# Optimization experiments

Measured on AMD Instinct MI355X. Metric: run time of the kernel, lower is better.

Reference implementation:

```python
import jax, jax.numpy as jnp
import numpy as np

GROUP = 32
HEADS = 8
EPS = 1e-5


def setup_inputs() -> dict:
    key = jax.random.key(0)
    k1, k2, k3 = jax.random.split(key, 3)
    C = 512
    x = jax.random.normal(k1, (8, C, 32, 32), dtype=jnp.float32)
    gn_w = jnp.ones((C,), dtype=jnp.float32)
    gn_b = jnp.zeros((C,), dtype=jnp.float32)
    # 1x1 convs == channel matmuls; init like torch conv default (kaiming-ish scale)
    w_qkv = jax.random.normal(k2, (3 * C, C), dtype=jnp.float32) * (1.0 / np.sqrt(C))
    w_proj = jax.random.normal(k3, (C, C), dtype=jnp.float32) * (1.0 / np.sqrt(C))
    return {"x": x, "gn_w": gn_w, "gn_b": gn_b, "w_qkv": w_qkv, "w_proj": w_proj}


def _forward(x, gn_w, gn_b, w_qkv, w_proj):
    B, C, H, W = x.shape
    N = H * W
    d = C // HEADS
    scale = d ** -0.5
    # GroupNorm over (channels_per_group, H, W)
    xg = x.reshape(B, GROUP, C // GROUP, H, W)
    mean = xg.mean(axis=(2, 3, 4), keepdims=True)
    var = xg.var(axis=(2, 3, 4), keepdims=True)
    xn = ((xg - mean) * jax.lax.rsqrt(var + EPS)).reshape(B, C, H, W)
    xn = xn * gn_w[None, :, None, None] + gn_b[None, :, None, None]
    # 1x1 conv QKV: [3C, C] x [B, C, H, W]
    qkv = jnp.einsum('oc,bchw->bohw', w_qkv, xn)
    q, k, v = jnp.split(qkv, 3, axis=1)

    def to_heads(t):  # b (h d) H W -> b h N d
        return t.reshape(B, HEADS, d, N).transpose(0, 1, 3, 2)

    q, k, v = to_heads(q), to_heads(k), to_heads(v)
    scores = jnp.einsum('bhid,bhjd->bhij', q, k) * scale
    probs = jax.nn.softmax(scores, axis=-1)
    out = jnp.einsum('bhij,bhjd->bhid', probs, v)
    # b h N d -> b (h d) H W
    out = out.transpose(0, 1, 3, 2).reshape(B, C, H, W)
    out = jnp.einsum('oc,bchw->bohw', w_proj, out)
    return x + out


def reference(x, gn_w, gn_b, w_qkv, w_proj):
    return _forward(x, gn_w, gn_b, w_qkv, w_proj)
```

## Files before the change

kernel.cpp:

```cpp
#include <hip/hip_runtime.h>

typedef __attribute__((ext_vector_type(4))) float f32x4;
typedef __attribute__((ext_vector_type(8))) __bf16 bf16x8;
typedef __attribute__((ext_vector_type(8))) unsigned short ushort8;

#define BATCH 8
#define CH    512
#define NN    1024
#define GRP   32
#define NHEAD 8
#define DH    64
#define QBLK  64
#define KBLK  64

static constexpr size_t OFF_STATS = 0;
static constexpr size_t OFF_WQB   = 4096;
static constexpr size_t OFF_WPB   = OFF_WQB + (size_t)1536*512*2;
static constexpr size_t OFF_XNT   = OFF_WPB + (size_t)512*512*2;
static constexpr size_t OFF_QKB   = OFF_XNT + (size_t)BATCH*NN*CH*2;
static constexpr size_t OFF_VT    = OFF_QKB + (size_t)BATCH*NN*1024*2;
static constexpr size_t OFF_ATTNT = OFF_VT  + (size_t)BATCH*CH*NN*2;

static __device__ __forceinline__ unsigned short f2bf(float f){
  union { float f; unsigned u; } cv; cv.f = f;
  unsigned u = cv.u;
  u += 0x7fffu + ((u >> 16) & 1u);
  return (unsigned short)(u >> 16);
}

static __device__ __forceinline__ unsigned pack2bf(float lo, float hi){
  union { __bf16 h[2]; unsigned u; } v;
  v.h[0] = (__bf16)lo; v.h[1] = (__bf16)hi;
  return v.u;
}

static __device__ __forceinline__ void gload_lds16(const unsigned short* g, unsigned short* l){
  __builtin_amdgcn_global_load_lds((const __attribute__((address_space(1))) void*)g,
                                   (__attribute__((address_space(3))) void*)l, 16, 0, 0);
}

__global__ __launch_bounds__(256) void pre_k(const float* __restrict__ x,
                                             const float* __restrict__ wq, const float* __restrict__ wp,
                                             float* __restrict__ stats,
                                             unsigned short* __restrict__ wqb, unsigned short* __restrict__ wpb){
  int bid = blockIdx.x;
  if (bid < 256){
    int bg = bid;
    const float4* base = (const float4*)(x + (size_t)bg * (16*NN));
    float s = 0.f, ss = 0.f;
    #pragma unroll 4
    for (int idx = threadIdx.x; idx < 16*NN/4; idx += 256){
      float4 v = base[idx];
      s  += (v.x + v.y) + (v.z + v.w);
      ss += (v.x*v.x + v.y*v.y) + (v.z*v.z + v.w*v.w);
    }
    for (int off = 32; off > 0; off >>= 1){ s += __shfl_down(s, off); ss += __shfl_down(ss, off); }
    __shared__ float red[8];
    int w = threadIdx.x >> 6, l = threadIdx.x & 63;
    if (l == 0){ red[w*2] = s; red[w*2+1] = ss; }
    __syncthreads();
    if (threadIdx.x == 0){
      float S  = red[0]+red[2]+red[4]+red[6];
      float SS = red[1]+red[3]+red[5]+red[7];
      float mean = S * (1.f/(16*NN));
      float var  = SS * (1.f/(16*NN)) - mean*mean;
      stats[bg*2]   = mean;
      stats[bg*2+1] = rsqrtf(var + 1e-5f);
    }
  } else {
    int i = (bid - 256)*256 + threadIdx.x;
    if (i < 1536*512) wqb[i] = f2bf(wq[i]);
    if (i < 512*512)  wpb[i] = f2bf(wp[i]);
  }
}

__global__ __launch_bounds__(256) void gn_apply_k(const float* __restrict__ x, const float* __restrict__ stats,
                                                  const float* __restrict__ gw, const float* __restrict__ gb,
                                                  unsigned short* __restrict__ xnT){
  int b = blockIdx.z, c0 = blockIdx.y*64, n0 = blockIdx.x*64;
  __shared__ unsigned short T[64][65];
  int t = threadIdx.x;
  int nl = t & 63;
  int cb = t >> 6;
  #pragma unroll
  for (int r = 0; r < 16; ++r){
    int cl = cb + r*4;
    int c  = c0 + cl;
    float xv   = x[((size_t)b*CH + c)*NN + n0 + nl];
    float mean = stats[(b*GRP + (c>>4))*2];
    float rstd = stats[(b*GRP + (c>>4))*2 + 1];
    float sc   = rstd * gw[c];
    T[cl][nl]  = f2bf((xv - mean)*sc + gb[c]);
  }
  __syncthreads();
  #pragma unroll
  for (int r = 0; r < 16; ++r){
    int nlocal = cb + r*4;
    xnT[((size_t)b*NN + n0 + nlocal)*CH + c0 + nl] = T[nl][nlocal];
  }
}

__global__ __launch_bounds__(256) void qkv_gemm_k(const unsigned short* __restrict__ wq,
                                                  const unsigned short* __restrict__ xnT,
                                                  unsigned short* __restrict__ qkb,
                                                  unsigned short* __restrict__ vT){
  int b  = blockIdx.z;
  int m0 = blockIdx.y * 128;
  int n0 = blockIdx.x * 128;
  __shared__ unsigned short As[128][64];
  __shared__ unsigned short Bs[128][64];
  int t = threadIdx.x;
  int w = t >> 6, l = t & 63;
  int wm = w >> 1, wn = w & 1;
  f32x4 acc[4][4] = {};
  const unsigned short* Ag = wq  + (size_t)(m0 + w*32)*512;
  const unsigned short* Bg = xnT + ((size_t)b*NN + n0 + w*32)*512;
  int r8 = l >> 3;
  int c8 = ((l & 7) ^ r8) * 8;
  int lr = l & 15, lg = l >> 4;
  int xr = (lr & 7) << 3;
  for (int k0 = 0; k0 < 512; k0 += 64){
    #pragma unroll
    for (int i = 0; i < 4; ++i){
      gload_lds16(Ag + (size_t)(i*8 + r8)*512 + k0 + c8, &As[w*32 + i*8][0]);
      gload_lds16(Bg + (size_t)(i*8 + r8)*512 + k0 + c8, &Bs[w*32 + i*8][0]);
    }
    __syncthreads();
    #pragma unroll
    for (int ks = 0; ks < 2; ++ks){
      bf16x8 af[4], bfr[4];
      #pragma unroll
      for (int mf = 0; mf < 4; ++mf) af[mf]  = *(const bf16x8*)&As[wm*64 + mf*16 + lr][(ks*32 + lg*8) ^ xr];
      #pragma unroll
      for (int nf = 0; nf < 4; ++nf) bfr[nf] = *(const bf16x8*)&Bs[wn*64 + nf*16 + lr][(ks*32 + lg*8) ^ xr];
      #pragma unroll
      for (int mf = 0; mf < 4; ++mf)
        #pragma unroll
        for (int nf = 0; nf < 4; ++nf)
          acc[mf][nf] = __builtin_amdgcn_mfma_f32_16x16x32_bf16(af[mf], bfr[nf], acc[mf][nf], 0, 0, 0);
    }
    __syncthreads();
  }
  int lq = l >> 4;
  float scl = (m0 < 512) ? 0.18033688f : 1.0f;
  if (m0 < 1024){
    #pragma unroll
    for (int mf = 0; mf < 4; ++mf)
      #pragma unroll
      for (int nf = 0; nf < 4; ++nf)
        #pragma unroll
        for (int r = 0; r < 4; ++r){
          int o = m0 + wm*64 + mf*16 + lq*4 + r;
          int n = n0 + wn*64 + nf*16 + lr;
          qkb[((size_t)b*NN + n)*1024 + o] = f2bf(acc[mf][nf][r] * scl);
        }
  } else {
    #pragma unroll
    for (int mf = 0; mf < 4; ++mf)
      #pragma unroll
      for (int nf = 0; nf < 4; ++nf)
        #pragma unroll
        for (int r = 0; r < 4; ++r){
          int o = m0 + wm*64 + mf*16 + lq*4 + r;
          int n = n0 + wn*64 + nf*16 + lr;
          vT[((size_t)b*512 + (o - 1024))*NN + n] = f2bf(acc[mf][nf][r]);
        }
  }
}

#define STAGE_KV(TT, BUF)                                                                \
  {                                                                                      \
    int jj = (TT) * KBLK;                                                                \
    _Pragma("unroll") for (int ch = 0; ch < 2; ++ch){                                    \
      gload_lds16(Kg + (size_t)(jj + w*16 + ch*8 + srow)*1024 + scol,                    \
                  &KV[0][BUF][w*16 + ch*8][0]);                                          \
      gload_lds16(Vg + (size_t)(w*16 + ch*8 + srow)*NN + jj + scol,                      \
                  &KV[1][BUF][w*16 + ch*8][0]);                                          \
    }                                                                                    \
  }

__global__ __launch_bounds__(256) void attn_k(const unsigned short* __restrict__ qkb,
                                              const unsigned short* __restrict__ vT,
                                              unsigned short* __restrict__ attnT){
  int bh = blockIdx.x;
  int b = bh >> 3, h = bh & 7;
  int q0 = blockIdx.y * QBLK;
  int t = threadIdx.x;
  int w = t >> 6, l = t & 63;
  int lr = l & 15, lg = l >> 4;

  __shared__ unsigned short KV[2][2][64][64];

  int srow = l >> 3;
  int scol = ((l & 7) ^ srow) * 8;
  const unsigned short* Kg = qkb + (size_t)b*NN*1024 + 512 + h*DH;
  const unsigned short* Vg = vT  + (size_t)(b*NHEAD + h)*DH*NN;

  bf16x8 qf[2];
  #pragma unroll
  for (int ks = 0; ks < 2; ++ks){
    int row = q0 + w*16 + lr;
    qf[ks] = *(const bf16x8*)(qkb + ((size_t)b*NN + row)*1024 + h*DH + ks*32 + lg*8);
  }

  float lsum = 0.f;
  f32x4 accO[4] = {};

  STAGE_KV(0, 0)
  __syncthreads();

  int xr = (lr & 7) * 8;
  int srcA = lr + ((lg & 1) << 5);
  int srcB = srcA + 16;
  bool hsel = (lg >> 1) != 0;

  for (int tt = 0; tt < 16; ++tt){
    int cur = tt & 1;
    if (tt < 15) STAGE_KV(tt + 1, cur ^ 1)
    bf16x8 kf[2][4], vf[2][4];
    #pragma unroll
    for (int ks = 0; ks < 2; ++ks)
      #pragma unroll
      for (int nf = 0; nf < 4; ++nf){
        kf[ks][nf] = *(const bf16x8*)&KV[0][cur][nf*16 + lr][(ks*32 + lg*8) ^ xr];
        vf[ks][nf] = *(const bf16x8*)&KV[1][cur][nf*16 + lr][(ks*32 + lg*8) ^ xr];
      }
    f32x4 sT[4] = {};
    __builtin_amdgcn_s_setprio(1);
    #pragma unroll
    for (int ks = 0; ks < 2; ++ks)
      #pragma unroll
      for (int nf = 0; nf < 4; ++nf)
        sT[nf] = __builtin_amdgcn_mfma_f32_16x16x32_bf16(kf[ks][nf], qf[ks], sT[nf], 0, 0, 0);
    __builtin_amdgcn_s_setprio(0);
    unsigned pk[4][2];
    #pragma unroll
    for (int nf = 0; nf < 4; ++nf){
      float p0 = exp2f(sT[nf][0]), p1 = exp2f(sT[nf][1]);
      float p2 = exp2f(sT[nf][2]), p3 = exp2f(sT[nf][3]);
      lsum += (p0 + p1) + (p2 + p3);
      pk[nf][0] = pack2bf(p0, p1);
      pk[nf][1] = pack2bf(p2, p3);
    }
    #pragma unroll
    for (int ks = 0; ks < 2; ++ks){
      unsigned a0 = (unsigned)__shfl((int)pk[2*ks  ][0], srcA);
      unsigned a1 = (unsigned)__shfl((int)pk[2*ks  ][1], srcA);
      unsigned a2 = (unsigned)__shfl((int)pk[2*ks  ][0], srcB);
      unsigned a3 = (unsigned)__shfl((int)pk[2*ks  ][1], srcB);
      unsigned b0 = (unsigned)__shfl((int)pk[2*ks+1][0], srcA);
      unsigned b1 = (unsigned)__shfl((int)pk[2*ks+1][1], srcA);
      unsigned b2 = (unsigned)__shfl((int)pk[2*ks+1][0], srcB);
      unsigned b3 = (unsigned)__shfl((int)pk[2*ks+1][1], srcB);
      union { unsigned u[4]; bf16x8 v; } pf;
      pf.u[0] = hsel ? b0 : a0;
      pf.u[1] = hsel ? b1 : a1;
      pf.u[2] = hsel ? b2 : a2;
      pf.u[3] = hsel ? b3 : a3;
      __builtin_amdgcn_s_setprio(1);
      #pragma unroll
      for (int nf = 0; nf < 4; ++nf)
        accO[nf] = __builtin_amdgcn_mfma_f32_16x16x32_bf16(vf[ks][nf], pf.v, accO[nf], 0, 0, 0);
      __builtin_amdgcn_s_setprio(0);
    }
    __syncthreads();
  }

  lsum += __shfl_xor(lsum, 16);
  lsum += __shfl_xor(lsum, 32);
  lsum = 1.f / lsum;

  unsigned short* Ob = &KV[0][0][0][0] + w * 1152;
  #pragma unroll
  for (int nf = 0; nf < 4; ++nf)
    #pragma unroll
    for (int r = 0; r < 4; ++r){
      __bf16 hv = (__bf16)(accO[nf][r] * lsum);
      Ob[lr*72 + nf*16 + lg*4 + r] = *(unsigned short*)&hv;
    }
  __syncthreads();
  int qr = l >> 2, cc = (l & 3) * 16;
  bf16x8 o0 = *(const bf16x8*)&Ob[qr*72 + cc];
  bf16x8 o1 = *(const bf16x8*)&Ob[qr*72 + cc + 8];
  unsigned short* dst = attnT + ((size_t)b*NN + q0 + w*16 + qr)*CH + h*DH + cc;
  *(bf16x8*)dst = o0;
  *(bf16x8*)(dst + 8) = o1;
}

__global__ __launch_bounds__(256) void proj_gemm_k(const unsigned short* __restrict__ wp,
                                                   const unsigned short* __restrict__ attnT,
                                                   const float* __restrict__ x, float* __restrict__ out){
  int b  = blockIdx.z;
  int m0 = blockIdx.y * 64;
  int n0 = blockIdx.x * 128;
  __shared__ unsigned short As[64][64];
  __shared__ unsigned short Bs[128][64];
  int t = threadIdx.x;
  int w = t >> 6, l = t & 63;
  int wm = w >> 1, wn = w & 1;
  f32x4 acc[2][4] = {};
  const unsigned short* Ag = wp    + (size_t)(m0 + w*16)*512;
  const unsigned short* Bg = attnT + ((size_t)b*NN + n0 + w*32)*512;
  int r8 = l >> 3;
  int c8 = ((l & 7) ^ r8) * 8;
  int lr = l & 15, lg = l >> 4;
  int xr = (lr & 7) << 3;
  for (int k0 = 0; k0 < 512; k0 += 64){
    #pragma unroll
    for (int i = 0; i < 2; ++i)
      gload_lds16(Ag + (size_t)(i*8 + r8)*512 + k0 + c8, &As[w*16 + i*8][0]);
    #pragma unroll
    for (int i = 0; i < 4; ++i)
      gload_lds16(Bg + (size_t)(i*8 + r8)*512 + k0 + c8, &Bs[w*32 + i*8][0]);
    __syncthreads();
    #pragma unroll
    for (int ks = 0; ks < 2; ++ks){
      bf16x8 af[2], bfr[4];
      #pragma unroll
      for (int mf = 0; mf < 2; ++mf) af[mf]  = *(const bf16x8*)&As[wm*32 + mf*16 + lr][(ks*32 + lg*8) ^ xr];
      #pragma unroll
      for (int nf = 0; nf < 4; ++nf) bfr[nf] = *(const bf16x8*)&Bs[wn*64 + nf*16 + lr][(ks*32 + lg*8) ^ xr];
      #pragma unroll
      for (int mf = 0; mf < 2; ++mf)
        #pragma unroll
        for (int nf = 0; nf < 4; ++nf)
          acc[mf][nf] = __builtin_amdgcn_mfma_f32_16x16x32_bf16(af[mf], bfr[nf], acc[mf][nf], 0, 0, 0);
    }
    __syncthreads();
  }
  int lq = l >> 4;
  #pragma unroll
  for (int mf = 0; mf < 2; ++mf)
    #pragma unroll
    for (int nf = 0; nf < 4; ++nf)
      #pragma unroll
      for (int r = 0; r < 4; ++r){
        int o = m0 + wm*32 + mf*16 + lq*4 + r;
        int n = n0 + wn*64 + nf*16 + lr;
        size_t idx = ((size_t)b*CH + o)*NN + n;
        out[idx] = x[idx] + acc[mf][nf][r];
      }
}

extern "C" void kernel_launch(void* const* d_in, const int* in_sizes, int n_in,
                              void* d_out, int out_size, void* d_ws, size_t ws_size,
                              hipStream_t stream){
  const float* x  = (const float*)d_in[0];
  const float* gw = (const float*)d_in[1];
  const float* gb = (const float*)d_in[2];
  const float* wq = (const float*)d_in[3];
  const float* wp = (const float*)d_in[4];
  float* out = (float*)d_out;
  char* ws = (char*)d_ws;
  float*          stats = (float*)(ws + OFF_STATS);
  unsigned short* wqb   = (unsigned short*)(ws + OFF_WQB);
  unsigned short* wpb   = (unsigned short*)(ws + OFF_WPB);
  unsigned short* xnT   = (unsigned short*)(ws + OFF_XNT);
  unsigned short* qkb   = (unsigned short*)(ws + OFF_QKB);
  unsigned short* vT    = (unsigned short*)(ws + OFF_VT);
  unsigned short* attnT = (unsigned short*)(ws + OFF_ATTNT);

  hipLaunchKernelGGL(pre_k,      dim3(3328),      dim3(256), 0, stream, x, wq, wp, stats, wqb, wpb);
  hipLaunchKernelGGL(gn_apply_k, dim3(16, 8, 8),  dim3(256), 0, stream, x, stats, gw, gb, xnT);
  hipLaunchKernelGGL(qkv_gemm_k, dim3(8, 12, 8),  dim3(256), 0, stream, wqb, xnT, qkb, vT);
  hipLaunchKernelGGL(attn_k,     dim3(64, 16),    dim3(256), 0, stream, qkb, vT, attnT);
  hipLaunchKernelGGL(proj_gemm_k,dim3(8, 8, 8),   dim3(256), 0, stream, wpb, attnT, x, out);
}
```

Measured before the change: 154.7 us.

## Switch attention to 32x32x16 MFMA with 128-row query blocks and permlane swaps

```diff
diff --git a/kernel.cpp b/kernel.cpp
--- a/kernel.cpp
+++ b/kernel.cpp
@@ -1,8 +1,9 @@
 #include <hip/hip_runtime.h>
 
-typedef __attribute__((ext_vector_type(4))) float f32x4;
-typedef __attribute__((ext_vector_type(8))) __bf16 bf16x8;
-typedef __attribute__((ext_vector_type(8))) unsigned short ushort8;
+typedef __attribute__((ext_vector_type(4)))  float f32x4;
+typedef __attribute__((ext_vector_type(16))) float f32x16;
+typedef __attribute__((ext_vector_type(8)))  __bf16 bf16x8;
+typedef __attribute__((ext_vector_type(8)))  unsigned short ushort8;
 
 #define BATCH 8
 #define CH    512
@@ -10,7 +11,7 @@
 #define GRP   32
 #define NHEAD 8
 #define DH    64
-#define QBLK  64
+#define QBLK  128
 #define KBLK  64
 
 static constexpr size_t OFF_STATS = 0;
@@ -32,6 +33,10 @@
   union { __bf16 h[2]; unsigned u; } v;
   v.h[0] = (__bf16)lo; v.h[1] = (__bf16)hi;
   return v.u;
+}
+
+static __device__ __forceinline__ void plswap(unsigned &a, unsigned &b){
+  asm("v_permlane32_swap_b32 %0, %1" : "+v"(a), "+v"(b));
 }
 
 static __device__ __forceinline__ void gload_lds16(const unsigned short* g, unsigned short* l){
@@ -187,7 +192,7 @@
   int q0 = blockIdx.y * QBLK;
   int t = threadIdx.x;
   int w = t >> 6, l = t & 63;
-  int lr = l & 15, lg = l >> 4;
+  int lo5 = l & 31, hi = l >> 5;
 
   __shared__ unsigned short KV[2][2][64][64];
 
@@ -196,95 +201,89 @@
   const unsigned short* Kg = qkb + (size_t)b*NN*1024 + 512 + h*DH;
   const unsigned short* Vg = vT  + (size_t)(b*NHEAD + h)*DH*NN;
 
-  bf16x8 qf[2];
-  #pragma unroll
-  for (int ks = 0; ks < 2; ++ks){
-    int row = q0 + w*16 + lr;
-    qf[ks] = *(const bf16x8*)(qkb + ((size_t)b*NN + row)*1024 + h*DH + ks*32 + lg*8);
-  }
+  bf16x8 qf[4];
+  #pragma unroll
+  for (int ks = 0; ks < 4; ++ks)
+    qf[ks] = *(const bf16x8*)(qkb + ((size_t)b*NN + q0 + w*32 + lo5)*1024 + h*DH + ks*16 + hi*8);
 
   float lsum = 0.f;
-  f32x4 accO[4] = {};
+  f32x16 accO[2] = {};
 
   STAGE_KV(0, 0)
   __syncthreads();
 
-  int xr = (lr & 7) * 8;
-  int srcA = lr + ((lg & 1) << 5);
-  int srcB = srcA + 16;
-  bool hsel = (lg >> 1) != 0;
+  int xr = (lo5 & 7) * 8;
 
   for (int tt = 0; tt < 16; ++tt){
     int cur = tt & 1;
     if (tt < 15) STAGE_KV(tt + 1, cur ^ 1)
-    bf16x8 kf[2][4], vf[2][4];
-    #pragma unroll
-    for (int ks = 0; ks < 2; ++ks)
-      #pragma unroll
-      for (int nf = 0; nf < 4; ++nf){
-        kf[ks][nf] = *(const bf16x8*)&KV[0][cur][nf*16 + lr][(ks*32 + lg*8) ^ xr];
-        vf[ks][nf] = *(const bf16x8*)&KV[1][cur][nf*16 + lr][(ks*32 + lg*8) ^ xr];
-      }
-    f32x4 sT[4] = {};
+
+    bf16x8 kf[2][4];
+    #pragma unroll
+    for (int f = 0; f < 2; ++f)
+      #pragma unroll
+      for (int ks = 0; ks < 4; ++ks)
+        kf[f][ks] = *(const bf16x8*)&KV[0][cur][f*32 + lo5][(ks*16 + hi*8) ^ xr];
+
+    f32x16 sT0 = {}, sT1 = {};
     __builtin_amdgcn_s_setprio(1);
     #pragma unroll
-    for (int ks = 0; ks < 2; ++ks)
-      #pragma unroll
-      for (int nf = 0; nf < 4; ++nf)
-        sT[nf] = __builtin_amdgcn_mfma_f32_16x16x32_bf16(kf[ks][nf], qf[ks], sT[nf], 0, 0, 0);
+    for (int ks = 0; ks < 4; ++ks)
+      sT0 = __builtin_amdgcn_mfma_f32_32x32x16_bf16(kf[0][ks], qf[ks], sT0, 0, 0, 0);
+    #pragma unroll
+    for (int ks = 0; ks < 4; ++ks)
+      sT1 = __builtin_amdgcn_mfma_f32_32x32x16_bf16(kf[1][ks], qf[ks], sT1, 0, 0, 0);
     __builtin_amdgcn_s_setprio(0);
-    unsigned pk[4][2];
-    #pragma unroll
-    for (int nf = 0; nf < 4; ++nf){
-      float p0 = exp2f(sT[nf][0]), p1 = exp2f(sT[nf][1]);
-      float p2 = exp2f(sT[nf][2]), p3 = exp2f(sT[nf][3]);
-      lsum += (p0 + p1) + (p2 + p3);
-      pk[nf][0] = pack2bf(p0, p1);
-      pk[nf][1] = pack2bf(p2, p3);
-    }
-    #pragma unroll
-    for (int ks = 0; ks < 2; ++ks){
-      unsigned a0 = (unsigned)__shfl((int)pk[2*ks  ][0], srcA);
-      unsigned a1 = (unsigned)__shfl((int)pk[2*ks  ][1], srcA);
-      unsigned a2 = (unsigned)__shfl((int)pk[2*ks  ][0], srcB);
-      unsigned a3 = (unsigned)__shfl((int)pk[2*ks  ][1], srcB);
-      unsigned b0 = (unsigned)__shfl((int)pk[2*ks+1][0], srcA);
-      unsigned b1 = (unsigned)__shfl((int)pk[2*ks+1][1], srcA);
-      unsigned b2 = (unsigned)__shfl((int)pk[2*ks+1][0], srcB);
-      unsigned b3 = (unsigned)__shfl((int)pk[2*ks+1][1], srcB);
+
+    bf16x8 vf[2][4];
+    #pragma unroll
+    for (int c = 0; c < 2; ++c)
+      #pragma unroll
+      for (int m = 0; m < 4; ++m)
+        vf[c][m] = *(const bf16x8*)&KV[1][cur][c*32 + lo5][(m*16 + hi*8) ^ xr];
+
+    float p0[16], p1[16];
+    #pragma unroll
+    for (int r = 0; r < 16; ++r){
+      p0[r] = exp2f(sT0[r]); lsum += p0[r];
+      p1[r] = exp2f(sT1[r]); lsum += p1[r];
+    }
+
+    #pragma unroll
+    for (int m = 0; m < 4; ++m){
+      const float* pv = (m < 2) ? p0 : p1;
+      int mm = (m & 1) * 8;
+      unsigned x1 = pack2bf(pv[mm+0], pv[mm+1]);
+      unsigned y1 = pack2bf(pv[mm+4], pv[mm+5]);
+      unsigned x2 = pack2bf(pv[mm+2], pv[mm+3]);
+      unsigned y2 = pack2bf(pv[mm+6], pv[mm+7]);
+      plswap(x1, y1);
+      plswap(x2, y2);
       union { unsigned u[4]; bf16x8 v; } pf;
-      pf.u[0] = hsel ? b0 : a0;
-      pf.u[1] = hsel ? b1 : a1;
-      pf.u[2] = hsel ? b2 : a2;
-      pf.u[3] = hsel ? b3 : a3;
+      pf.u[0] = x1; pf.u[1] = x2; pf.u[2] = y1; pf.u[3] = y2;
       __builtin_amdgcn_s_setprio(1);
-      #pragma unroll
-      for (int nf = 0; nf < 4; ++nf)
-        accO[nf] = __builtin_amdgcn_mfma_f32_16x16x32_bf16(vf[ks][nf], pf.v, accO[nf], 0, 0, 0);
+      accO[0] = __builtin_amdgcn_mfma_f32_32x32x16_bf16(pf.v, vf[0][m], accO[0], 0, 0, 0);
+      accO[1] = __builtin_amdgcn_mfma_f32_32x32x16_bf16(pf.v, vf[1][m], accO[1], 0, 0, 0);
       __builtin_amdgcn_s_setprio(0);
     }
     __syncthreads();
   }
 
-  lsum += __shfl_xor(lsum, 16);
   lsum += __shfl_xor(lsum, 32);
-  lsum = 1.f / lsum;
-
-  unsigned short* Ob = &KV[0][0][0][0] + w * 1152;
-  #pragma unroll
-  for (int nf = 0; nf < 4; ++nf)
-    #pragma unroll
-    for (int r = 0; r < 4; ++r){
-      __bf16 hv = (__bf16)(accO[nf][r] * lsum);
-      Ob[lr*72 + nf*16 + lg*4 + r] = *(unsigned short*)&hv;
-    }
-  __syncthreads();
-  int qr = l >> 2, cc = (l & 3) * 16;
-  bf16x8 o0 = *(const bf16x8*)&Ob[qr*72 + cc];
-  bf16x8 o1 = *(const bf16x8*)&Ob[qr*72 + cc + 8];
-  unsigned short* dst = attnT + ((size_t)b*NN + q0 + w*16 + qr)*CH + h*DH + cc;
-  *(bf16x8*)dst = o0;
-  *(bf16x8*)(dst + 8) = o1;
+  float inv = 1.f / lsum;
+
+  float invq[16];
+  #pragma unroll
+  for (int r = 0; r < 16; ++r)
+    invq[r] = __shfl(inv, (r & 3) + 8*(r >> 2) + 4*hi);
+
+  #pragma unroll
+  for (int r = 0; r < 16; ++r){
+    int qr = (r & 3) + 8*(r >> 2) + 4*hi;
+    unsigned short* dst = attnT + ((size_t)b*NN + q0 + w*32 + qr)*CH + h*DH + lo5;
+    dst[0]  = f2bf(accO[0][r] * invq[r]);
+    dst[32] = f2bf(accO[1][r] * invq[r]);
+  }
 }
 
 __global__ __launch_bounds__(256) void proj_gemm_k(const unsigned short* __restrict__ wp,
@@ -363,6 +362,6 @@
   hipLaunchKernelGGL(pre_k,      dim3(3328),      dim3(256), 0, stream, x, wq, wp, stats, wqb, wpb);
   hipLaunchKernelGGL(gn_apply_k, dim3(16, 8, 8),  dim3(256), 0, stream, x, stats, gw, gb, xnT);
   hipLaunchKernelGGL(qkv_gemm_k, dim3(8, 12, 8),  dim3(256), 0, stream, wqb, xnT, qkb, vT);
-  hipLaunchKernelGGL(attn_k,     dim3(64, 16),    dim3(256), 0, stream, qkb, vT, attnT);
+  hipLaunchKernelGGL(attn_k,     dim3(64, 8),     dim3(256), 0, stream, qkb, vT, attnT);
   hipLaunchKernelGGL(proj_gemm_k,dim3(8, 8, 8),   dim3(256), 0, stream, wpb, attnT, x, out);
 }
```

Measured after the change: 147.7 us. 4.5% less time.
